# Kernel optimization log

Measured on AMD Instinct MI355X. Metric: run time of the kernel, lower is better.

The kernel has to match this reference:

```python
import jax, jax.numpy as jnp
import numpy as np

B, T, DV, H, DW, V, MAXLEN = 64, 32, 2048, 1024, 512, 20000, 3


def setup_inputs() -> dict:
    key = jax.random.key(0)
    ks = jax.random.split(key, 14)
    s = 1.0 / np.sqrt(H)

    def rn(k, shape, scale):
        return jax.random.normal(k, shape, jnp.float32) * scale

    return {
        "vid_feats": jax.random.normal(ks[0], (B, T, DV), jnp.float32),
        "W_ih1": rn(ks[1], (3 * H, DV), s),
        "W_hh1": rn(ks[2], (3 * H, H), s),
        "b_ih1": rn(ks[3], (3 * H,), s),
        "b_hh1": rn(ks[4], (3 * H,), s),
        "W_ih2": rn(ks[5], (3 * H, H + DW), s),
        "W_hh2": rn(ks[6], (3 * H, H), s),
        "b_ih2": rn(ks[7], (3 * H,), s),
        "b_hh2": rn(ks[8], (3 * H,), s),
        "W_obj": rn(ks[9], (V, H), s),
        "b_obj": rn(ks[10], (V,), s),
        "W_rel": rn(ks[11], (V, H), s),
        "b_rel": rn(ks[12], (V,), s),
    }


def _gru_cell(x_proj, h, W_hh, b_hh):
    # PyTorch GRU gate math. x_proj = x @ W_ih.T + b_ih (precomputed).
    hp = h @ W_hh.T + b_hh
    xr, xz, xn = jnp.split(x_proj, 3, axis=-1)
    hr, hz, hn = jnp.split(hp, 3, axis=-1)
    r = jax.nn.sigmoid(xr + hr)
    z = jax.nn.sigmoid(xz + hz)
    n = jnp.tanh(xn + r * hn)
    return (1.0 - z) * n + z * h


def reference(vid_feats, W_ih1, W_hh1, b_ih1, b_hh1,
              W_ih2, W_hh2, b_ih2, b_hh2,
              W_obj, b_obj, W_rel, b_rel):
    Bsz = vid_feats.shape[0]
    Hh = W_hh1.shape[1]
    dtype = vid_feats.dtype

    # ---- encoder: rnn1 over video frames (input projection batched) ----
    xp1 = jnp.einsum('btd,gd->btg', vid_feats, W_ih1) + b_ih1  # [B,T,3H]

    def step1(h, xp):
        h = _gru_cell(xp, h, W_hh1, b_hh1)
        return h, h

    h1, out1 = jax.lax.scan(step1, jnp.zeros((Bsz, Hh), dtype),
                            jnp.swapaxes(xp1, 0, 1))  # out1: [T,B,H]

    # ---- rnn2 over concat(out1, zero word embeddings): zero part drops out ----
    W_ih2_h = W_ih2[:, :Hh]  # columns multiplying the hidden part
    xp2 = jnp.einsum('tbh,gh->tbg', out1, W_ih2_h) + b_ih2  # [T,B,3H]

    def step2(h, xp):
        return _gru_cell(xp, h, W_hh2, b_hh2), None

    h2, _ = jax.lax.scan(step2, jnp.zeros((Bsz, Hh), dtype), xp2)

    # ---- decode loop: zero frame / zero word inputs each step ----
    xp1_pad = jnp.broadcast_to(b_ih1, (Bsz, b_ih1.shape[0]))
    probs = []
    for i in range(MAXLEN):
        h1 = _gru_cell(xp1_pad, h1, W_hh1, b_hh1)
        xp2_t = h1 @ W_ih2_h.T + b_ih2
        h2 = _gru_cell(xp2_t, h2, W_hh2, b_hh2)
        if i != 1:
            logits = h2 @ W_obj.T + b_obj
        else:
            logits = h2 @ W_rel.T + b_rel
        probs.append(jax.nn.log_softmax(logits, axis=-1))
    return jnp.stack(probs, axis=1)  # [B, MAXLEN, V]
```

## Files before the change

### kernel.cpp

```cpp
#include <hip/hip_runtime.h>
#include <math.h>

#define Bsz 64
#define Tt  32
#define TTOT 35
#define Dv  2048
#define Hd  1024
#define G3  3072
#define Vv  20000
#define ML  3
#define NTILE 1250

typedef __attribute__((ext_vector_type(8))) short bf16x8;
typedef __attribute__((ext_vector_type(4))) float f32x4;
typedef unsigned long long u64;
#define MFMA(a,b,c) __builtin_amdgcn_mfma_f32_16x16x32_bf16(a,b,c,0,0,0)

__device__ __forceinline__ short f2bf(float f) {
    union { float f; unsigned u; } v; v.f = f;
    unsigned r = v.u + 0x7fffu + ((v.u >> 16) & 1u);
    return (short)(r >> 16);
}
__device__ __forceinline__ void cvt8(const float* __restrict__ s,
                                     short* __restrict__ d) {
    float4 x = *(const float4*)s;
    float4 y = *(const float4*)(s + 4);
    bf16x8 o;
    o[0]=f2bf(x.x); o[1]=f2bf(x.y); o[2]=f2bf(x.z); o[3]=f2bf(x.w);
    o[4]=f2bf(y.x); o[5]=f2bf(y.y); o[6]=f2bf(y.z); o[7]=f2bf(y.w);
    *(bf16x8*)d = o;
}
__device__ __forceinline__ bf16x8 pack8(const float* __restrict__ s) {
    float4 x = *(const float4*)s;
    float4 y = *(const float4*)(s + 4);
    bf16x8 o;
    o[0]=f2bf(x.x); o[1]=f2bf(x.y); o[2]=f2bf(x.z); o[3]=f2bf(x.w);
    o[4]=f2bf(y.x); o[5]=f2bf(y.y); o[6]=f2bf(y.z); o[7]=f2bf(y.w);
    return o;
}

__device__ __forceinline__ void poll_flags(const unsigned* fl, unsigned tgt) {
    const int lane = threadIdx.x & 63;
    unsigned f = __hip_atomic_load(&fl[lane], __ATOMIC_RELAXED,
                                   __HIP_MEMORY_SCOPE_AGENT);
    while (!__all((int)(f >= tgt))) {
        __builtin_amdgcn_s_sleep(2);
        f = __hip_atomic_load(&fl[lane], __ATOMIC_RELAXED,
                              __HIP_MEMORY_SCOPE_AGENT);
    }
}

__global__ __launch_bounds__(256)
void cvt2(const float* __restrict__ vid,  short* __restrict__ vid_bf,
          const float* __restrict__ Wih1, short* __restrict__ Wih1_bf)
{
    const long b0 = 524288;
    const long b1 = b0 + 786432;
    for (long i = (long)blockIdx.x * 256 + threadIdx.x; i < b1;
         i += (long)gridDim.x * 256) {
        if (i < b0) cvt8(vid + i * 8, vid_bf + i * 8);
        else { const long q = i - b0; cvt8(Wih1 + q * 8, Wih1_bf + q * 8); }
    }
}

__global__ __launch_bounds__(256, 1)
void mega(const short* __restrict__ vid_bf, const short* __restrict__ Wih1_bf,
          const float* __restrict__ b_ih1, float* __restrict__ xp1,
          const float* __restrict__ Whh1f, const float* __restrict__ b_hh1,
          const float* __restrict__ Wih2f, const float* __restrict__ b_ih2,
          const float* __restrict__ Whh2f, const float* __restrict__ b_hh2,
          short* __restrict__ out1h,
          float* __restrict__ xp2s,
          short* __restrict__ h2h,
          unsigned* __restrict__ flags1, unsigned* __restrict__ flagsP,
          unsigned* __restrict__ flags2, unsigned* __restrict__ flagsG)
{
    __shared__ __align__(16) short Wl[4 * 3 * 8 * 64 * 8];
    __shared__ __align__(16) float xch[4][4][3][256];
    __shared__ __align__(16) short hstage[64][16];
    const int tid = threadIdx.x;
    const int w  = tid >> 6;
    const int l  = tid & 63;
    const int lr = l & 15, lg = l >> 4;
    const int role = blockIdx.x >> 6;
    const int k    = blockIdx.x & 63;

    if (role == 3) {
        short* As = Wl;
        short* Bs = Wl + 128 * 40;
        const int wm = w >> 1, wn = w & 1;
        const int sm = tid >> 2;
        const int skg = tid & 3;
        for (int jj = 0; jj < 6; ++jj) {
            const int job = k + jj * 64;
            const int mt0 = job / 24, nt0 = job % 24;
            const int m0 = mt0 * 128, n0 = nt0 * 128;
            f32x4 acc[4][4] = {};
            for (int k0 = 0; k0 < Dv; k0 += 32) {
                #pragma unroll
                for (int i = 0; i < 2; ++i) {
                    const int m = m0 + i * 64 + sm;
                    const int arow = (m & 63) * Tt + (m >> 6);
                    bf16x8 av = *(const bf16x8*)(vid_bf + (size_t)arow * Dv + k0 + skg * 8);
                    bf16x8 wv = *(const bf16x8*)(Wih1_bf + (size_t)(n0 + i * 64 + sm) * Dv + k0 + skg * 8);
                    *(bf16x8*)(As + (i * 64 + sm) * 40 + skg * 8) = av;
                    *(bf16x8*)(Bs + (i * 64 + sm) * 40 + skg * 8) = wv;
                }
                __syncthreads();
                bf16x8 af[4], bfr[4];
                #pragma unroll
                for (int mt = 0; mt < 4; ++mt) {
                    af[mt]  = *(const bf16x8*)(As + (wm * 64 + mt * 16 + lr) * 40 + lg * 8);
                    bfr[mt] = *(const bf16x8*)(Bs + (wn * 64 + mt * 16 + lr) * 40 + lg * 8);
                }
                #pragma unroll
                for (int mt = 0; mt < 4; ++mt)
                    #pragma unroll
                    for (int nt = 0; nt < 4; ++nt)
                        acc[mt][nt] = MFMA(af[mt], bfr[nt], acc[mt][nt]);
                __syncthreads();
            }
            #pragma unroll
            for (int mt = 0; mt < 4; ++mt)
                #pragma unroll
                for (int nt = 0; nt < 4; ++nt)
                    #pragma unroll
                    for (int v = 0; v < 4; ++v) {
                        const int m = m0 + wm * 64 + mt * 16 + lg * 4 + v;
                        const int n = n0 + wn * 64 + nt * 16 + lr;
                        union { float f; unsigned u; } cv;
                        cv.f = acc[mt][nt][v] + b_ih1[n];
                        __hip_atomic_store((unsigned*)(xp1 + (size_t)m * G3 + n),
                                           cv.u, __ATOMIC_RELAXED,
                                           __HIP_MEMORY_SCOPE_AGENT);
                    }
            __syncthreads();
            if (tid == 0)
                __hip_atomic_fetch_add(&flagsG[mt0], 1u, __ATOMIC_RELAXED,
                                       __HIP_MEMORY_SCOPE_AGENT);
        }
        return;
    }

    const int j0 = k * 16;
    const int j  = j0 + lr;
    const float* Wf = (role == 0) ? Whh1f : (role == 1) ? Wih2f : Whh2f;
    const int ldw   = (role == 1) ? (Hd + 512) : Hd;
    const float* bias = (role == 0) ? b_hh1 : (role == 1) ? b_ih2 : b_hh2;

    #pragma unroll
    for (int g = 0; g < 3; ++g)
        #pragma unroll
        for (int ks = 0; ks < 8; ++ks) {
            const float* src = Wf + (size_t)(g * Hd + j) * ldw + w * 256 + ks * 32 + lg * 8;
            *(bf16x8*)(Wl + ((((w * 3 + g) * 8 + ks) * 64) + l) * 8) = pack8(src);
        }

    const float b0 = bias[j], b1 = bias[Hd + j], b2 = bias[2 * Hd + j];
    short* Ab = (role == 2) ? h2h : out1h;

    float bxr = 0.f, bxz = 0.f, bxn = 0.f;
    if (role == 0) {
        bxr = b_ih1[j]; bxz = b_ih1[Hd + j]; bxn = b_ih1[2 * Hd + j];
    }
    float hp[4] = {0.f, 0.f, 0.f, 0.f};
    float xr[4], xz[4], xn[4];
    __syncthreads();

    for (int t = 0; t < TTOT; ++t) {
        if (role == 0) {
            if (w == 0) poll_flags(flags1, (unsigned)t);
            else if (w == 2 && t < Tt) {
                const unsigned* fg = &flagsG[t >> 1];
                while (__hip_atomic_load(fg, __ATOMIC_RELAXED,
                                         __HIP_MEMORY_SCOPE_AGENT) < 24u)
                    __builtin_amdgcn_s_sleep(2);
            }
        } else if (role == 1) {
            if (w == 0) poll_flags(flags1, (unsigned)(t + 1));
        } else {
            if (w == 0)      poll_flags(flagsP, (unsigned)(t + 1));
            else if (w == 1) poll_flags(flags2, (unsigned)t);
        }
        __syncthreads();
        asm volatile("" ::: "memory");

        const short* hin = Ab + (size_t)(role == 1 ? t + 1 : t) * (64 * Hd);
        bf16x8 A[4][8];
        #pragma unroll
        for (int mt = 0; mt < 4; ++mt)
            #pragma unroll
            for (int ks = 0; ks < 8; ++ks)
                A[mt][ks] = *(const bf16x8*)(hin + (size_t)(mt * 16 + lr) * Hd
                                             + w * 256 + ks * 32 + lg * 8);
        if (role == 0) {
            if (t < Tt) {
                #pragma unroll
                for (int v = 0; v < 4; ++v) {
                    const int b = w * 16 + lg * 4 + v;
                    const float* xrow = xp1 + (size_t)(t * 64 + b) * G3;
                    xr[v] = xrow[j]; xz[v] = xrow[Hd + j]; xn[v] = xrow[2 * Hd + j];
                }
            } else {
                #pragma unroll
                for (int v = 0; v < 4; ++v) { xr[v]=bxr; xz[v]=bxz; xn[v]=bxn; }
            }
        } else if (role == 2) {
            #pragma unroll
            for (int v = 0; v < 4; ++v) {
                const int b = w * 16 + lg * 4 + v;
                const float* xrow = xp2s + ((size_t)t * 64 + b) * G3;
                xr[v] = xrow[j]; xz[v] = xrow[Hd + j]; xn[v] = xrow[2 * Hd + j];
            }
        }

        f32x4 acc[4][3] = {};
        #pragma unroll
        for (int ks = 0; ks < 8; ++ks) {
            bf16x8 B0 = *(const bf16x8*)(Wl + ((((w * 3 + 0) * 8 + ks) * 64) + l) * 8);
            bf16x8 B1 = *(const bf16x8*)(Wl + ((((w * 3 + 1) * 8 + ks) * 64) + l) * 8);
            bf16x8 B2 = *(const bf16x8*)(Wl + ((((w * 3 + 2) * 8 + ks) * 64) + l) * 8);
            #pragma unroll
            for (int mt = 0; mt < 4; ++mt) {
                acc[mt][0] = MFMA(A[mt][ks], B0, acc[mt][0]);
                acc[mt][1] = MFMA(A[mt][ks], B1, acc[mt][1]);
                acc[mt][2] = MFMA(A[mt][ks], B2, acc[mt][2]);
            }
        }

        #pragma unroll
        for (int mt = 0; mt < 4; ++mt)
            #pragma unroll
            for (int g = 0; g < 3; ++g)
                *(f32x4*)&xch[w][mt][g][l * 4] = acc[mt][g];
        __syncthreads();
        f32x4 tot[3];
        #pragma unroll
        for (int g = 0; g < 3; ++g) {
            f32x4 t0 = *(const f32x4*)&xch[0][w][g][l * 4];
            f32x4 t1 = *(const f32x4*)&xch[1][w][g][l * 4];
            f32x4 t2 = *(const f32x4*)&xch[2][w][g][l * 4];
            f32x4 t3 = *(const f32x4*)&xch[3][w][g][l * 4];
            tot[g] = (t0 + t1) + (t2 + t3);
        }

        if (role == 1) {
            const float bg[3] = {b0, b1, b2};
            #pragma unroll
            for (int v = 0; v < 4; ++v) {
                const int b = w * 16 + lg * 4 + v;
                #pragma unroll
                for (int g = 0; g < 3; ++g) {
                    union { float f; unsigned u; } cv;
                    cv.f = tot[g][v] + bg[g];
                    __hip_atomic_store(
                        (unsigned*)(xp2s + ((size_t)t * 64 + b) * G3 + g * Hd + j),
                        cv.u, __ATOMIC_RELAXED, __HIP_MEMORY_SCOPE_AGENT);
                }
            }
            __syncthreads();
        } else {
            #pragma unroll
            for (int v = 0; v < 4; ++v) {
                const int b = w * 16 + lg * 4 + v;
                const float rg = 1.f / (1.f + __expf(-(xr[v] + tot[0][v] + b0)));
                const float zg = 1.f / (1.f + __expf(-(xz[v] + tot[1][v] + b1)));
                const float ng = tanhf(xn[v] + rg * (tot[2][v] + b2));
                const float hv = (1.f - zg) * ng + zg * hp[v];
                hp[v] = hv;
                hstage[b][lr] = f2bf(hv);
            }
            __syncthreads();
            {
                const int b = tid >> 2, part = tid & 3;
                const u64 pv = *(const u64*)&hstage[b][part * 4];
                __hip_atomic_store(
                    (u64*)(Ab + (size_t)(t + 1) * (64 * Hd) + b * Hd + j0 + part * 4),
                    pv, __ATOMIC_RELAXED, __HIP_MEMORY_SCOPE_AGENT);
            }
            __syncthreads();
        }

        if (tid == 0) {
            unsigned* fl = (role == 0) ? flags1 : (role == 1) ? flagsP : flags2;
            __hip_atomic_store(&fl[k], (unsigned)(t + 1),
                               __ATOMIC_RELAXED, __HIP_MEMORY_SCOPE_AGENT);
        }
    }
}

__global__ __launch_bounds__(256)
void logits_dual(const short* __restrict__ h2h,
                 const float* __restrict__ Wobj, const float* __restrict__ bobj,
                 const float* __restrict__ Wrel, const float* __restrict__ brel,
                 float* __restrict__ logits3)
{
    const int tid = threadIdx.x;
    const int w = tid >> 6, l = tid & 63;
    const int lr = l & 15, lg = l >> 4;
    const bool dual = blockIdx.x < 313;
    const int nb = dual ? blockIdx.x : blockIdx.x - 313;
    const int tile = nb * 4 + w;
    if (tile >= NTILE) return;
    const int n0 = tile * 16;
    const float* Wo = dual ? Wobj : Wrel;
    const float* bo = dual ? bobj : brel;
    const short* hA = h2h + (size_t)33 * 64 * Hd;
    const short* hB = h2h + (size_t)34 * 64 * Hd;
    const short* hC = h2h + (size_t)35 * 64 * Hd;

    f32x4 accA[4] = {}, accC[4] = {};
    const float* wbase = Wo + (size_t)(n0 + lr) * Hd + lg * 8;
    #pragma unroll 4
    for (int ks = 0; ks < 32; ++ks) {
        const bf16x8 wv = pack8(wbase + ks * 32);
        if (dual) {
            #pragma unroll
            for (int mt = 0; mt < 4; ++mt) {
                bf16x8 a = *(const bf16x8*)(hA + (size_t)(mt * 16 + lr) * Hd + ks * 32 + lg * 8);
                bf16x8 c = *(const bf16x8*)(hC + (size_t)(mt * 16 + lr) * Hd + ks * 32 + lg * 8);
                accA[mt] = MFMA(a, wv, accA[mt]);
                accC[mt] = MFMA(c, wv, accC[mt]);
            }
        } else {
            #pragma unroll
            for (int mt = 0; mt < 4; ++mt) {
                bf16x8 a = *(const bf16x8*)(hB + (size_t)(mt * 16 + lr) * Hd + ks * 32 + lg * 8);
                accA[mt] = MFMA(a, wv, accA[mt]);
            }
        }
    }

    const float bn = bo[n0 + lr];
    float* lg0 = logits3 + (size_t)(dual ? 0 : 1) * 64 * Vv;
    float* lg2 = logits3 + (size_t)2 * 64 * Vv;
    #pragma unroll
    for (int mt = 0; mt < 4; ++mt)
        #pragma unroll
        for (int v = 0; v < 4; ++v) {
            const size_t row = (size_t)(mt * 16 + lg * 4 + v) * Vv + n0 + lr;
            lg0[row] = accA[mt][v] + bn;
            if (dual) lg2[row] = accC[mt][v] + bn;
        }
}

__global__ __launch_bounds__(256)
void log_softmax_all(const float* __restrict__ logits3, float* __restrict__ out)
{
    __shared__ float red[4];
    const int step = blockIdx.x >> 6;
    const int b    = blockIdx.x & 63;
    const int tid  = threadIdx.x;
    const float* row = logits3 + ((size_t)step * 64 + b) * Vv;

    float m = -1e30f;
    for (int v = tid; v < Vv; v += 256) m = fmaxf(m, row[v]);
    #pragma unroll
    for (int off = 32; off > 0; off >>= 1) m = fmaxf(m, __shfl_down(m, off, 64));
    if ((tid & 63) == 0) red[tid >> 6] = m;
    __syncthreads();
    m = fmaxf(fmaxf(red[0], red[1]), fmaxf(red[2], red[3]));
    __syncthreads();

    float s = 0.f;
    for (int v = tid; v < Vv; v += 256) s += expf(row[v] - m);
    #pragma unroll
    for (int off = 32; off > 0; off >>= 1) s += __shfl_down(s, off, 64);
    if ((tid & 63) == 0) red[tid >> 6] = s;
    __syncthreads();
    s = red[0] + red[1] + red[2] + red[3];
    const float lse = m + logf(s);

    float* orow = out + ((size_t)b * ML + step) * Vv;
    for (int v = tid; v < Vv; v += 256) orow[v] = row[v] - lse;
}

extern "C" void kernel_launch(void* const* d_in, const int* in_sizes, int n_in,
                              void* d_out, int out_size, void* d_ws, size_t ws_size,
                              hipStream_t stream)
{
    (void)in_sizes; (void)n_in; (void)out_size; (void)ws_size;
    const float* vid   = (const float*)d_in[0];
    const float* W_ih1 = (const float*)d_in[1];
    const float* W_hh1 = (const float*)d_in[2];
    const float* b_ih1 = (const float*)d_in[3];
    const float* b_hh1 = (const float*)d_in[4];
    const float* W_ih2 = (const float*)d_in[5];
    const float* W_hh2 = (const float*)d_in[6];
    const float* b_ih2 = (const float*)d_in[7];
    const float* b_hh2 = (const float*)d_in[8];
    const float* W_obj = (const float*)d_in[9];
    const float* b_obj = (const float*)d_in[10];
    const float* W_rel = (const float*)d_in[11];
    const float* b_rel = (const float*)d_in[12];
    float* out = (float*)d_out;

    char* p = (char*)d_ws;
    short* vid_bf   = (short*)p; p += (size_t)2048 * Dv * 2;
    short* Wih1_bf  = (short*)p; p += (size_t)G3 * Dv * 2;
    unsigned int* flg = (unsigned int*)p; p += 4096;
    short* out1h  = (short*)p; p += (size_t)36 * 64 * Hd * 2;
    short* h2h    = (short*)p; p += (size_t)36 * 64 * Hd * 2;
    float* xp1    = (float*)p; p += (size_t)2048 * G3 * 4;
    float* xp2s   = (float*)p; p += (size_t)TTOT * 64 * G3 * 4;
    float* logits3= (float*)p; p += (size_t)ML * 64 * Vv * 4;

    unsigned* flags1 = flg;
    unsigned* flagsP = flg + 64;
    unsigned* flags2 = flg + 128;
    unsigned* flagsG = flg + 192;

    hipMemsetAsync(flg, 0, 4096, stream);
    hipMemsetAsync(out1h, 0, (size_t)64 * Hd * 2, stream);
    hipMemsetAsync(h2h,   0, (size_t)64 * Hd * 2, stream);

    cvt2<<<640, 256, 0, stream>>>(vid, vid_bf, W_ih1, Wih1_bf);

    mega<<<256, 256, 0, stream>>>(
        vid_bf, Wih1_bf, b_ih1, xp1,
        W_hh1, b_hh1, W_ih2, b_ih2, W_hh2, b_hh2,
        out1h, xp2s, h2h, flags1, flagsP, flags2, flagsG);

    logits_dual<<<626, 256, 0, stream>>>(h2h, W_obj, b_obj, W_rel, b_rel, logits3);

    log_softmax_all<<<192, 256, 0, stream>>>(logits3, out);
}
```

Before: 554.8 us.

## Split input-projection GEMM out of persistent GRU kernel and prefetch logits weights

Moves the xp1 input-projection GEMM out of the persistent recurrent kernel into a separate full-grid kernel (384 blocks, fragment-ordered LDS layout). This drops the flag-based overlap between GEMM and recurrence, and the GRU kernel shrinks to 192 blocks. The next step's xp1 values are now prefetched right after the gate update, hiding that load latency. The logits kernel gains a two-deep register prefetch of fp32 weights with a merged MFMA path. The trade-off is that the GEMM no longer overlaps the early recurrence steps, while it gains full-GPU parallelism and the recurrence loses the GEMM polling waits.

```diff
diff --git a/kernel.cpp b/kernel.cpp
--- a/kernel.cpp
+++ b/kernel.cpp
@@ -38,6 +38,12 @@
     o[4]=f2bf(y.x); o[5]=f2bf(y.y); o[6]=f2bf(y.z); o[7]=f2bf(y.w);
     return o;
 }
+__device__ __forceinline__ bf16x8 pack2(const float4& x, const float4& y) {
+    bf16x8 o;
+    o[0]=f2bf(x.x); o[1]=f2bf(x.y); o[2]=f2bf(x.z); o[3]=f2bf(x.w);
+    o[4]=f2bf(y.x); o[5]=f2bf(y.y); o[6]=f2bf(y.z); o[7]=f2bf(y.w);
+    return o;
+}
 
 __device__ __forceinline__ void poll_flags(const unsigned* fl, unsigned tgt) {
     const int lane = threadIdx.x & 63;
@@ -63,9 +69,65 @@
     }
 }
 
+__global__ __launch_bounds__(256)
+void gemm_xp1(const short* __restrict__ vid_bf,
+              const short* __restrict__ Wih1_bf,
+              const float* __restrict__ b_ih1,
+              float* __restrict__ xp1)
+{
+    __shared__ __align__(16) short As[8 * 64 * 8];
+    __shared__ __align__(16) short Bs[8 * 64 * 8];
+    const int tid = threadIdx.x;
+    const int w = tid >> 6, l = tid & 63;
+    const int wm = w >> 1, wn = w & 1;
+    const int lr = l & 15, lg = l >> 4;
+    const int m0 = blockIdx.y * 128, n0 = blockIdx.x * 128;
+    const int sr = tid >> 2;
+    const int sc = tid & 3;
+
+    f32x4 acc[4][4] = {};
+
+    for (int k0 = 0; k0 < Dv; k0 += 32) {
+        #pragma unroll
+        for (int i = 0; i < 2; ++i) {
+            const int r = i * 64 + sr;
+            const int m = m0 + r;
+            const int arow = (m & 63) * Tt + (m >> 6);
+            bf16x8 av = *(const bf16x8*)(vid_bf + (size_t)arow * Dv + k0 + sc * 8);
+            bf16x8 bv = *(const bf16x8*)(Wih1_bf + (size_t)(n0 + r) * Dv + k0 + sc * 8);
+            const int fi = (r >> 4) * 64 + sc * 16 + (r & 15);
+            *(bf16x8*)(As + fi * 8) = av;
+            *(bf16x8*)(Bs + fi * 8) = bv;
+        }
+        __syncthreads();
+        bf16x8 af[4], bfr[4];
+        #pragma unroll
+        for (int mt = 0; mt < 4; ++mt) {
+            af[mt]  = *(const bf16x8*)(As + ((wm * 4 + mt) * 64 + l) * 8);
+            bfr[mt] = *(const bf16x8*)(Bs + ((wn * 4 + mt) * 64 + l) * 8);
+        }
+        #pragma unroll
+        for (int mt = 0; mt < 4; ++mt)
+            #pragma unroll
+            for (int nt = 0; nt < 4; ++nt)
+                acc[mt][nt] = MFMA(af[mt], bfr[nt], acc[mt][nt]);
+        __syncthreads();
+    }
+
+    #pragma unroll
+    for (int mt = 0; mt < 4; ++mt)
+        #pragma unroll
+        for (int nt = 0; nt < 4; ++nt)
+            #pragma unroll
+            for (int v = 0; v < 4; ++v) {
+                const int m = m0 + wm * 64 + mt * 16 + lg * 4 + v;
+                const int n = n0 + wn * 64 + nt * 16 + lr;
+                xp1[(size_t)m * G3 + n] = acc[mt][nt][v] + b_ih1[n];
+            }
+}
+
 __global__ __launch_bounds__(256, 1)
-void mega(const short* __restrict__ vid_bf, const short* __restrict__ Wih1_bf,
-          const float* __restrict__ b_ih1, float* __restrict__ xp1,
+void mega(const float* __restrict__ xp1, const float* __restrict__ b_ih1,
           const float* __restrict__ Whh1f, const float* __restrict__ b_hh1,
           const float* __restrict__ Wih2f, const float* __restrict__ b_ih2,
           const float* __restrict__ Whh2f, const float* __restrict__ b_hh2,
@@ -73,7 +135,7 @@
           float* __restrict__ xp2s,
           short* __restrict__ h2h,
           unsigned* __restrict__ flags1, unsigned* __restrict__ flagsP,
-          unsigned* __restrict__ flags2, unsigned* __restrict__ flagsG)
+          unsigned* __restrict__ flags2)
 {
     __shared__ __align__(16) short Wl[4 * 3 * 8 * 64 * 8];
     __shared__ __align__(16) float xch[4][4][3][256];
@@ -84,66 +146,9 @@
     const int lr = l & 15, lg = l >> 4;
     const int role = blockIdx.x >> 6;
     const int k    = blockIdx.x & 63;
-
-    if (role == 3) {
-        short* As = Wl;
-        short* Bs = Wl + 128 * 40;
-        const int wm = w >> 1, wn = w & 1;
-        const int sm = tid >> 2;
-        const int skg = tid & 3;
-        for (int jj = 0; jj < 6; ++jj) {
-            const int job = k + jj * 64;
-            const int mt0 = job / 24, nt0 = job % 24;
-            const int m0 = mt0 * 128, n0 = nt0 * 128;
-            f32x4 acc[4][4] = {};
-            for (int k0 = 0; k0 < Dv; k0 += 32) {
-                #pragma unroll
-                for (int i = 0; i < 2; ++i) {
-                    const int m = m0 + i * 64 + sm;
-                    const int arow = (m & 63) * Tt + (m >> 6);
-                    bf16x8 av = *(const bf16x8*)(vid_bf + (size_t)arow * Dv + k0 + skg * 8);
-                    bf16x8 wv = *(const bf16x8*)(Wih1_bf + (size_t)(n0 + i * 64 + sm) * Dv + k0 + skg * 8);
-                    *(bf16x8*)(As + (i * 64 + sm) * 40 + skg * 8) = av;
-                    *(bf16x8*)(Bs + (i * 64 + sm) * 40 + skg * 8) = wv;
-                }
-                __syncthreads();
-                bf16x8 af[4], bfr[4];
-                #pragma unroll
-                for (int mt = 0; mt < 4; ++mt) {
-                    af[mt]  = *(const bf16x8*)(As + (wm * 64 + mt * 16 + lr) * 40 + lg * 8);
-                    bfr[mt] = *(const bf16x8*)(Bs + (wn * 64 + mt * 16 + lr) * 40 + lg * 8);
-                }
-                #pragma unroll
-                for (int mt = 0; mt < 4; ++mt)
-                    #pragma unroll
-                    for (int nt = 0; nt < 4; ++nt)
-                        acc[mt][nt] = MFMA(af[mt], bfr[nt], acc[mt][nt]);
-                __syncthreads();
-            }
-            #pragma unroll
-            for (int mt = 0; mt < 4; ++mt)
-                #pragma unroll
-                for (int nt = 0; nt < 4; ++nt)
-                    #pragma unroll
-                    for (int v = 0; v < 4; ++v) {
-                        const int m = m0 + wm * 64 + mt * 16 + lg * 4 + v;
-                        const int n = n0 + wn * 64 + nt * 16 + lr;
-                        union { float f; unsigned u; } cv;
-                        cv.f = acc[mt][nt][v] + b_ih1[n];
-                        __hip_atomic_store((unsigned*)(xp1 + (size_t)m * G3 + n),
-                                           cv.u, __ATOMIC_RELAXED,
-                                           __HIP_MEMORY_SCOPE_AGENT);
-                    }
-            __syncthreads();
-            if (tid == 0)
-                __hip_atomic_fetch_add(&flagsG[mt0], 1u, __ATOMIC_RELAXED,
-                                       __HIP_MEMORY_SCOPE_AGENT);
-        }
-        return;
-    }
-
     const int j0 = k * 16;
     const int j  = j0 + lr;
+
     const float* Wf = (role == 0) ? Whh1f : (role == 1) ? Wih2f : Whh2f;
     const int ldw   = (role == 1) ? (Hd + 512) : Hd;
     const float* bias = (role == 0) ? b_hh1 : (role == 1) ? b_ih2 : b_hh2;
@@ -160,25 +165,23 @@
     short* Ab = (role == 2) ? h2h : out1h;
 
     float bxr = 0.f, bxz = 0.f, bxn = 0.f;
+    float hp[4] = {0.f, 0.f, 0.f, 0.f};
+    float xr[4], xz[4], xn[4];
     if (role == 0) {
         bxr = b_ih1[j]; bxz = b_ih1[Hd + j]; bxn = b_ih1[2 * Hd + j];
-    }
-    float hp[4] = {0.f, 0.f, 0.f, 0.f};
-    float xr[4], xz[4], xn[4];
+        #pragma unroll
+        for (int v = 0; v < 4; ++v) {
+            const int b = w * 16 + lg * 4 + v;
+            const float* xrow = xp1 + (size_t)b * G3;
+            xr[v] = xrow[j]; xz[v] = xrow[Hd + j]; xn[v] = xrow[2 * Hd + j];
+        }
+    }
     __syncthreads();
 
     for (int t = 0; t < TTOT; ++t) {
-        if (role == 0) {
-            if (w == 0) poll_flags(flags1, (unsigned)t);
-            else if (w == 2 && t < Tt) {
-                const unsigned* fg = &flagsG[t >> 1];
-                while (__hip_atomic_load(fg, __ATOMIC_RELAXED,
-                                         __HIP_MEMORY_SCOPE_AGENT) < 24u)
-                    __builtin_amdgcn_s_sleep(2);
-            }
-        } else if (role == 1) {
-            if (w == 0) poll_flags(flags1, (unsigned)(t + 1));
-        } else {
+        if (role == 0)      { if (w == 0) poll_flags(flags1, (unsigned)t); }
+        else if (role == 1) { if (w == 0) poll_flags(flags1, (unsigned)(t + 1)); }
+        else {
             if (w == 0)      poll_flags(flagsP, (unsigned)(t + 1));
             else if (w == 1) poll_flags(flags2, (unsigned)t);
         }
@@ -193,19 +196,7 @@
             for (int ks = 0; ks < 8; ++ks)
                 A[mt][ks] = *(const bf16x8*)(hin + (size_t)(mt * 16 + lr) * Hd
                                              + w * 256 + ks * 32 + lg * 8);
-        if (role == 0) {
-            if (t < Tt) {
-                #pragma unroll
-                for (int v = 0; v < 4; ++v) {
-                    const int b = w * 16 + lg * 4 + v;
-                    const float* xrow = xp1 + (size_t)(t * 64 + b) * G3;
-                    xr[v] = xrow[j]; xz[v] = xrow[Hd + j]; xn[v] = xrow[2 * Hd + j];
-                }
-            } else {
-                #pragma unroll
-                for (int v = 0; v < 4; ++v) { xr[v]=bxr; xz[v]=bxz; xn[v]=bxn; }
-            }
-        } else if (role == 2) {
+        if (role == 2) {
             #pragma unroll
             for (int v = 0; v < 4; ++v) {
                 const int b = w * 16 + lg * 4 + v;
@@ -269,6 +260,19 @@
                 const float hv = (1.f - zg) * ng + zg * hp[v];
                 hp[v] = hv;
                 hstage[b][lr] = f2bf(hv);
+            }
+            if (role == 0) {
+                if (t + 1 < Tt) {
+                    #pragma unroll
+                    for (int v = 0; v < 4; ++v) {
+                        const int b = w * 16 + lg * 4 + v;
+                        const float* xrow = xp1 + (size_t)((t + 1) * 64 + b) * G3;
+                        xr[v] = xrow[j]; xz[v] = xrow[Hd + j]; xn[v] = xrow[2 * Hd + j];
+                    }
+                } else {
+                    #pragma unroll
+                    for (int v = 0; v < 4; ++v) { xr[v]=bxr; xz[v]=bxz; xn[v]=bxn; }
+                }
             }
             __syncthreads();
             {
@@ -308,27 +312,37 @@
     const short* hA = h2h + (size_t)33 * 64 * Hd;
     const short* hB = h2h + (size_t)34 * 64 * Hd;
     const short* hC = h2h + (size_t)35 * 64 * Hd;
+    const short* h0 = dual ? hA : hB;
 
     f32x4 accA[4] = {}, accC[4] = {};
     const float* wbase = Wo + (size_t)(n0 + lr) * Hd + lg * 8;
-    #pragma unroll 4
+
+    float4 wx[2], wy[2];
+    wx[0] = *(const float4*)(wbase);          wy[0] = *(const float4*)(wbase + 4);
+    wx[1] = *(const float4*)(wbase + 32);     wy[1] = *(const float4*)(wbase + 36);
+
+    #pragma unroll
     for (int ks = 0; ks < 32; ++ks) {
-        const bf16x8 wv = pack8(wbase + ks * 32);
+        const int bi = ks & 1;
+        float4 nx = {}, ny = {};
+        if (ks < 30) {
+            nx = *(const float4*)(wbase + (ks + 2) * 32);
+            ny = *(const float4*)(wbase + (ks + 2) * 32 + 4);
+        }
+        const bf16x8 wv = pack2(wx[bi], wy[bi]);
+        #pragma unroll
+        for (int mt = 0; mt < 4; ++mt) {
+            bf16x8 a = *(const bf16x8*)(h0 + (size_t)(mt * 16 + lr) * Hd + ks * 32 + lg * 8);
+            accA[mt] = MFMA(a, wv, accA[mt]);
+        }
         if (dual) {
             #pragma unroll
             for (int mt = 0; mt < 4; ++mt) {
-                bf16x8 a = *(const bf16x8*)(hA + (size_t)(mt * 16 + lr) * Hd + ks * 32 + lg * 8);
                 bf16x8 c = *(const bf16x8*)(hC + (size_t)(mt * 16 + lr) * Hd + ks * 32 + lg * 8);
-                accA[mt] = MFMA(a, wv, accA[mt]);
                 accC[mt] = MFMA(c, wv, accC[mt]);
             }
-        } else {
-            #pragma unroll
-            for (int mt = 0; mt < 4; ++mt) {
-                bf16x8 a = *(const bf16x8*)(hB + (size_t)(mt * 16 + lr) * Hd + ks * 32 + lg * 8);
-                accA[mt] = MFMA(a, wv, accA[mt]);
-            }
-        }
+        }
+        if (ks < 30) { wx[bi] = nx; wy[bi] = ny; }
     }
 
     const float bn = bo[n0 + lr];
@@ -408,7 +422,6 @@
     unsigned* flags1 = flg;
     unsigned* flagsP = flg + 64;
     unsigned* flags2 = flg + 128;
-    unsigned* flagsG = flg + 192;
 
     hipMemsetAsync(flg, 0, 4096, stream);
     hipMemsetAsync(out1h, 0, (size_t)64 * Hd * 2, stream);
@@ -416,10 +429,12 @@
 
     cvt2<<<640, 256, 0, stream>>>(vid, vid_bf, W_ih1, Wih1_bf);
 
-    mega<<<256, 256, 0, stream>>>(
-        vid_bf, Wih1_bf, b_ih1, xp1,
-        W_hh1, b_hh1, W_ih2, b_ih2, W_hh2, b_hh2,
-        out1h, xp2s, h2h, flags1, flagsP, flags2, flagsG);
+    gemm_xp1<<<dim3(G3 / 128, 2048 / 128), 256, 0, stream>>>(
+        vid_bf, Wih1_bf, b_ih1, xp1);
+
+    mega<<<192, 256, 0, stream>>>(
+        xp1, b_ih1, W_hh1, b_hh1, W_ih2, b_ih2, W_hh2, b_hh2,
+        out1h, xp2s, h2h, flags1, flagsP, flags2);
 
     logits_dual<<<626, 256, 0, stream>>>(h2h, W_obj, b_obj, W_rel, b_rel, logits3);
 
```

New measurement: 524.6 us. 5.5% less time.
